# Kernel tuning notes

Measured on AMD Instinct MI355X. Metric: run time of the kernel, lower is better.

The kernel has to match this reference:

```python
import jax, jax.numpy as jnp
import numpy as np

ODE_STEPS = 4
LN_EPS = 1e-5


def setup_inputs() -> dict:
    key = jax.random.key(0)
    ks = jax.random.split(key, 18)
    B, L, F, E, H, OH = 256, 1024, 64, 128, 128, 128
    s = lambda n: 1.0 / np.sqrt(n)
    u = lambda k, shp, n: jax.random.uniform(k, shp, jnp.float32, -s(n), s(n))
    return {
        "x": jax.random.normal(ks[0], (B, L, F), jnp.float32),
        "dt": jax.random.uniform(ks[1], (B, L), jnp.float32),
        "mask": jax.random.randint(ks[2], (B, L), 0, 2).astype(jnp.int32),
        # x_proj
        "Wx": u(ks[3], (E, F), F), "bx": u(ks[4], (E,), F),
        # ODEFunc: Linear(H,OH) -> tanh -> Linear(OH,H)
        "W1": u(ks[5], (OH, H), H), "b1": u(ks[6], (OH,), H),
        "W2": u(ks[7], (H, OH), OH), "b2": u(ks[8], (H,), OH),
        # GRUCell
        "W_ih": u(ks[9], (3 * H, E), H), "b_ih": u(ks[10], (3 * H,), H),
        "W_hh": u(ks[11], (3 * H, H), H), "b_hh": u(ks[12], (3 * H,), H),
        # head: LayerNorm + Linear(H,1)
        "ln_g": jnp.ones((H,), jnp.float32), "ln_b": jnp.zeros((H,), jnp.float32),
        "Wh": u(ks[13], (1, H), H), "bh": u(ks[14], (1,), H),
    }


def reference(x, dt, Wx, bx, W1, b1, W2, b2, W_ih, b_ih, W_hh, b_hh,
              ln_g, ln_b, Wh, bh, mask):
    B, L, F = x.shape
    H = W_hh.shape[1]

    def odefunc(h):
        return jnp.tanh(h @ W1.T + b1) @ W2.T + b2

    def ode_euler(h, dte):  # dte: [B]
        step = dte / float(ODE_STEPS)
        for _ in range(ODE_STEPS):
            h = h + step[:, None] * odefunc(h)
        return h

    def gru_cell(xe, h):
        gi = xe @ W_ih.T + b_ih
        gh = h @ W_hh.T + b_hh
        i_r, i_z, i_n = jnp.split(gi, 3, axis=-1)
        h_r, h_z, h_n = jnp.split(gh, 3, axis=-1)
        r = jax.nn.sigmoid(i_r + h_r)
        z = jax.nn.sigmoid(i_z + h_z)
        n = jnp.tanh(i_n + r * h_n)
        return (1.0 - z) * n + z * h

    def step(h, inp):
        xi, dti, mi = inp  # [B,F], [B], [B] int
        mi_f = mi.astype(x.dtype)
        active = jnp.sum(mi_f) > 0  # torch skips step only if ALL masked
        hi = ode_euler(h, dti * mi_f)
        xe = jax.nn.relu(xi @ Wx.T + bx)
        hg = gru_cell(xe, hi)
        h_new = jnp.where(active, hg, h)
        return h_new, h_new

    h0 = jnp.zeros((B, H), x.dtype)
    xs = (jnp.swapaxes(x, 0, 1), dt.T, mask.T)
    _, Hs = jax.lax.scan(step, h0, xs)       # [L,B,H]
    Hs = jnp.swapaxes(Hs, 0, 1)              # [B,L,H]

    mu = jnp.mean(Hs, axis=-1, keepdims=True)
    var = jnp.var(Hs, axis=-1, keepdims=True)
    hn = (Hs - mu) / jnp.sqrt(var + LN_EPS) * ln_g + ln_b
    logits_t = (hn @ Wh.T + bh)[..., 0]      # [B,L]

    mask_f = mask.astype(x.dtype)
    logits_t = logits_t * mask_f
    len_valid = jnp.maximum(jnp.sum(mask_f, axis=1), 1.0)
    return jnp.sum(logits_t, axis=1) / len_valid
```

## Files before the change

### kernel.cpp

```cpp
#include <hip/hip_runtime.h>

#define Bb 256
#define Ll 1024
#define CH 32

typedef _Float16 h2v __attribute__((ext_vector_type(2)));

__device__ __forceinline__ unsigned pack_h2(float a, float b) {
  h2v v; v[0] = (_Float16)a; v[1] = (_Float16)b;
  return __builtin_bit_cast(unsigned, v);
}
__device__ __forceinline__ float dot2(unsigned w, unsigned x, float acc) {
#if defined(__has_builtin) && __has_builtin(__builtin_amdgcn_fdot2)
  return __builtin_amdgcn_fdot2(__builtin_bit_cast(h2v, w),
                                __builtin_bit_cast(h2v, x), acc, false);
#else
  h2v wv = __builtin_bit_cast(h2v, w), xv = __builtin_bit_cast(h2v, x);
  acc = fmaf((float)wv[0], (float)xv[0], acc);
  return fmaf((float)wv[1], (float)xv[1], acc);
#endif
}
__device__ __forceinline__ float dppadd1(float v) {
  int s = __builtin_amdgcn_mov_dpp(__builtin_bit_cast(int, v), 0xB1, 0xF, 0xF, true);
  return v + __builtin_bit_cast(float, s);
}
__device__ __forceinline__ float dppadd2(float v) {
  int s = __builtin_amdgcn_mov_dpp(__builtin_bit_cast(int, v), 0x4E, 0xF, 0xF, true);
  return v + __builtin_bit_cast(float, s);
}
__device__ __forceinline__ float qsum(float a0, float a1) {
  return dppadd2(dppadd1(a0 + a1));
}
__device__ __forceinline__ float fast_tanh(float x) {
  float e = __expf(2.0f * x);
  return 1.0f - 2.0f / (e + 1.0f);
}
__device__ __forceinline__ float fast_sigmoid(float x) {
  return 1.0f / (1.0f + __expf(-x));
}

__device__ __forceinline__ float mv16(const unsigned* __restrict__ w,
                                      const unsigned* __restrict__ v, int q0) {
  float a0 = 0.0f, a1 = 0.0f;
#pragma unroll
  for (int c = 0; c < 4; ++c) {
    const uint4 hv = *(const uint4*)&v[q0 + 4 * c];
    a0 = dot2(w[4*c+0], hv.x, a0); a1 = dot2(w[4*c+1], hv.y, a1);
    a0 = dot2(w[4*c+2], hv.z, a0); a1 = dot2(w[4*c+3], hv.w, a1);
  }
  return qsum(a0, a1);
}
__device__ __forceinline__ float giq(const unsigned* __restrict__ wrow,
                                     const unsigned* __restrict__ xe,
                                     int q0, int swi) {
  float g0 = 0.0f, g1 = 0.0f;
#pragma unroll
  for (int c = 0; c < 4; ++c) {
    const uint4 xv = *(const uint4*)&xe[q0 + 4 * c];
    const uint4 w4 = *(const uint4*)&wrow[(q0 + 4 * c) ^ swi];
    g0 = dot2(w4.x, xv.x, g0); g1 = dot2(w4.y, xv.y, g1);
    g0 = dot2(w4.z, xv.z, g0); g1 = dot2(w4.w, xv.w, g1);
  }
  return qsum(g0, g1);
}

__global__ __launch_bounds__(256) void k_prep(
    const float* __restrict__ W1, const float* __restrict__ W2,
    const float* __restrict__ b2, float* __restrict__ ws)
{
  const int idx = blockIdx.x * 256 + threadIdx.x;
  if (idx < 16384) {
    const int i = idx >> 7, j = idx & 127;
    float s = 0.f;
    for (int k = 0; k < 128; ++k) s = fmaf(W1[i * 128 + k], W2[k * 128 + j], s);
    ws[idx] = s;
  } else if (idx < 16512) {
    const int i = idx - 16384;
    float s = 0.f;
    for (int k = 0; k < 128; ++k) s = fmaf(W1[i * 128 + k], b2[k], s);
    ws[idx] = s;
  }
}

__global__ __launch_bounds__(512, 1) void k_fused(
    const float* __restrict__ x, const float* __restrict__ dtp,
    const int* __restrict__ mask,
    const float* __restrict__ Wx, const float* __restrict__ bx,
    const float* __restrict__ W1, const float* __restrict__ b1,
    const float* __restrict__ W2, const float* __restrict__ b2,
    const float* __restrict__ Wih, const float* __restrict__ bih,
    const float* __restrict__ Whh, const float* __restrict__ bhh,
    const float* __restrict__ lng, const float* __restrict__ lnb,
    const float* __restrict__ Whd, const float* __restrict__ bhp,
    const float* __restrict__ ws,
    float* __restrict__ out)
{
  const float* Mf = ws;
  const float* cf = ws + 16384;

  const int b = blockIdx.x;
  const int tid = threadIdx.x;
  const int lane = tid & 63;
  const int wv = tid >> 6;
  const int jl = lane >> 2;
  const int ks = lane & 3;
  const int j = (wv << 4) + jl;
  const int q0 = ks << 4;
  const int q0x = ks << 3;
  const int swi = (j & 15) << 2;

  __shared__ int act_lds[Ll];
  __shared__ __align__(16) unsigned wih_lds[3 * 128 * 64];
  __shared__ __align__(16) unsigned w2_lds[128 * 64];
  __shared__ __align__(16) unsigned x16[2][CH * 32];
  __shared__ __align__(16) unsigned xe16[64];
  __shared__ __align__(16) unsigned ubuf[2][64];
  __shared__ __align__(16) unsigned usumb[64];
  __shared__ __align__(16) unsigned fb16[64];
  __shared__ __align__(16) unsigned h16[2][64];
  __shared__ float dt_ch[2][CH];
  __shared__ int   m_ch[2][CH];
  __shared__ float red_lds[48];
  __shared__ float cc_lds[2];

  for (int t0 = tid; t0 < Ll; t0 += 512) {
    int a = 0;
#pragma unroll 8
    for (int bb = 0; bb < Bb; ++bb) a |= mask[(size_t)bb * Ll + t0];
    act_lds[t0] = a;
  }
  for (int idx = tid; idx < 3 * 128 * 64; idx += 512) {
    const int r = idx >> 6, w = idx & 63;
    wih_lds[(r << 6) | (w ^ ((r & 15) << 2))] =
        pack_h2(Wih[(size_t)r * 128 + 2 * w], Wih[(size_t)r * 128 + 2 * w + 1]);
  }
  for (int idx = tid; idx < 128 * 64; idx += 512) {
    const int r = idx >> 6, w = idx & 63;
    w2_lds[(r << 6) | (w ^ ((r & 15) << 2))] =
        pack_h2(W2[(size_t)r * 128 + 2 * w], W2[(size_t)r * 128 + 2 * w + 1]);
  }
  if (tid == 0) {
    float s1 = 0.f, s0 = 0.f;
    for (int i = 0; i < 128; ++i) { s1 += lng[i] * Whd[i]; s0 += lnb[i] * Whd[i]; }
    cc_lds[0] = s1; cc_lds[1] = s0 + bhp[0];
  }
  {
    const int sl = tid >> 4, part = tid & 15;
    const float4 a = *(const float4*)(x + ((size_t)b * Ll + sl) * 64 + part * 4);
    x16[0][sl * 32 + part * 2 + 0] = pack_h2(a.x, a.y);
    x16[0][sl * 32 + part * 2 + 1] = pack_h2(a.z, a.w);
    if (tid < CH) dt_ch[0][tid] = dtp[(size_t)b * Ll + tid];
    else if (tid < 2 * CH) m_ch[0][tid - CH] = mask[(size_t)b * Ll + (tid - CH)];
  }
  unsigned w1h[16], mh[16], whr[16], whz[16], whn[16], wxh[8];
#pragma unroll
  for (int ii = 0; ii < 8; ++ii) {
    float4 a4;
    a4 = *(const float4*)&W1[(size_t)j * 128 + (ks << 5) + 4 * ii];
    w1h[2*ii] = pack_h2(a4.x, a4.y); w1h[2*ii+1] = pack_h2(a4.z, a4.w);
    a4 = *(const float4*)&Mf[(size_t)j * 128 + (ks << 5) + 4 * ii];
    mh[2*ii] = pack_h2(a4.x, a4.y); mh[2*ii+1] = pack_h2(a4.z, a4.w);
    a4 = *(const float4*)&Whh[(size_t)j * 128 + (ks << 5) + 4 * ii];
    whr[2*ii] = pack_h2(a4.x, a4.y); whr[2*ii+1] = pack_h2(a4.z, a4.w);
    a4 = *(const float4*)&Whh[(size_t)(128 + j) * 128 + (ks << 5) + 4 * ii];
    whz[2*ii] = pack_h2(a4.x, a4.y); whz[2*ii+1] = pack_h2(a4.z, a4.w);
    a4 = *(const float4*)&Whh[(size_t)(256 + j) * 128 + (ks << 5) + 4 * ii];
    whn[2*ii] = pack_h2(a4.x, a4.y); whn[2*ii+1] = pack_h2(a4.z, a4.w);
  }
#pragma unroll
  for (int ii = 0; ii < 4; ++ii) {
    const float4 a4 = *(const float4*)&Wx[(size_t)j * 64 + (ks << 4) + 4 * ii];
    wxh[2*ii] = pack_h2(a4.x, a4.y); wxh[2*ii+1] = pack_h2(a4.z, a4.w);
  }
  const float bxj = bx[j], b1j = b1[j], b2j = b2[j], cj = cf[j];
  const float bir = bih[j], biz = bih[128 + j], bin_ = bih[256 + j];
  const float bhr = bhh[j], bhz = bhh[128 + j], bhn = bhh[256 + j];
  const float gw = lng[j] * Whd[j];

  if (tid < 64) { h16[0][tid] = 0u; h16[1][tid] = 0u; }
  float hreg = 0.f;
  float gicr = 0.f, gicz = 0.f, gicn = 0.f;
  float gnr = 0.f, gnz = 0.f, gnn = 0.f;
  float accb = 0.f, cntb = 0.f;
  int mreg = 0;
  float4 rx0 = {0,0,0,0}; float rdt = 0.f; int rmk = 0;
  __syncthreads();

  {
    float p0 = 0.f, p1 = 0.f;
#pragma unroll
    for (int c = 0; c < 2; ++c) {
      const uint4 xv = *(const uint4*)&x16[0][q0x + 4 * c];
      p0 = dot2(wxh[4*c+0], xv.x, p0); p1 = dot2(wxh[4*c+1], xv.y, p1);
      p0 = dot2(wxh[4*c+2], xv.z, p0); p1 = dot2(wxh[4*c+3], xv.w, p1);
    }
    const float xev = fmaxf(qsum(p0, p1) + bxj, 0.f);
    if (ks == 0) ((_Float16*)xe16)[j] = (_Float16)xev;
  }
  __syncthreads();
  gicr = giq(&wih_lds[j << 6], xe16, q0, swi) + bir;
  gicz = giq(&wih_lds[(128 + j) << 6], xe16, q0, swi) + biz;
  gicn = giq(&wih_lds[(256 + j) << 6], xe16, q0, swi) + bin_;
  __syncthreads();

#pragma unroll 1
  for (int t = 0; t < Ll; ++t) {
    const int cb = (t >> 5) & 1, tc = t & 31;
    const float sv = dt_ch[cb][tc] * (float)m_ch[cb][tc] * 0.25f;
    const unsigned* hb = h16[t & 1];
    const int refill = (tc == 16) && ((t >> 5) < 31);

    float v, usum;

    {
      if (refill) {
        const int sl = tid >> 4, part = tid & 15;
        rx0 = *(const float4*)(x + ((size_t)b * Ll + ((t >> 5) + 1) * 32 + sl) * 64 + part * 4);
        if (tid < CH) rdt = dtp[(size_t)b * Ll + ((t >> 5) + 1) * 32 + tid];
        else if (tid < 2 * CH) rmk = mask[(size_t)b * Ll + ((t >> 5) + 1) * 32 + (tid - CH)];
      }
      v = mv16(w1h, hb, q0);
      const float u0 = fast_tanh(v + b1j);
      usum = u0;
      if (ks == 0) ((_Float16*)ubuf[0])[j] = (_Float16)u0;
      if (t + 1 < Ll) {
        const int nb2 = ((t + 1) >> 5) & 1, ns = (t + 1) & 31;
        float p0 = 0.f, p1 = 0.f;
#pragma unroll
        for (int c = 0; c < 2; ++c) {
          const uint4 xv = *(const uint4*)&x16[nb2][ns * 32 + q0x + 4 * c];
          p0 = dot2(wxh[4*c+0], xv.x, p0); p1 = dot2(wxh[4*c+1], xv.y, p1);
          p0 = dot2(wxh[4*c+2], xv.z, p0); p1 = dot2(wxh[4*c+3], xv.w, p1);
        }
        const float xev = fmaxf(qsum(p0, p1) + bxj, 0.f);
        if (ks == 0) ((_Float16*)xe16)[j] = (_Float16)xev;
      }
      if (tid == 0 && t > 0) {
        float S1 = 0.f, S2 = 0.f, SD = 0.f;
#pragma unroll
        for (int q = 0; q < 16; ++q) {
          S1 += red_lds[q * 3 + 0]; S2 += red_lds[q * 3 + 1]; SD += red_lds[q * 3 + 2];
        }
        if (mreg) {
          const float mu = S1 * (1.0f / 128.0f);
          const float var = S2 * (1.0f / 128.0f) - mu * mu;
          const float rstd = rsqrtf(var + 1e-5f);
          accb += rstd * (SD - mu * cc_lds[0]) + cc_lds[1];
          cntb += 1.f;
        }
      }
    }
    __syncthreads();

    {
      const float t2 = mv16(mh, ubuf[0], q0);
      v = fmaf(sv, t2 + cj, v);
      const float u1 = fast_tanh(v + b1j);
      usum += u1;
      if (ks == 0) ((_Float16*)ubuf[1])[j] = (_Float16)u1;
      gnr = giq(&wih_lds[j << 6], xe16, q0, swi) + bir;
    }
    __syncthreads();

    {
      const float t2 = mv16(mh, ubuf[1], q0);
      v = fmaf(sv, t2 + cj, v);
      const float u2 = fast_tanh(v + b1j);
      usum += u2;
      if (ks == 0) ((_Float16*)ubuf[0])[j] = (_Float16)u2;
      gnz = giq(&wih_lds[(128 + j) << 6], xe16, q0, swi) + biz;
    }
    __syncthreads();

    {
      const float t2 = mv16(mh, ubuf[0], q0);
      v = fmaf(sv, t2 + cj, v);
      const float u3 = fast_tanh(v + b1j);
      usum += u3;
      if (ks == 0) ((_Float16*)usumb)[j] = (_Float16)usum;
      gnn = giq(&wih_lds[(256 + j) << 6], xe16, q0, swi) + bin_;
    }
    __syncthreads();

    float hf;
    {
      const float k2 = giq(&w2_lds[j << 6], usumb, q0, swi);
      hf = hreg + sv * k2 + 4.f * sv * b2j;
      if (ks == 0) ((_Float16*)fb16)[j] = (_Float16)hf;
      if (refill) {
        const int nb = ((t >> 5) + 1) & 1;
        const int sl = tid >> 4, part = tid & 15;
        x16[nb][sl * 32 + part * 2 + 0] = pack_h2(rx0.x, rx0.y);
        x16[nb][sl * 32 + part * 2 + 1] = pack_h2(rx0.z, rx0.w);
        if (tid < CH) dt_ch[nb][tid] = rdt;
        else if (tid < 2 * CH) m_ch[nb][tid - CH] = rmk;
      }
    }
    __syncthreads();

    {
      const float pr = mv16(whr, fb16, q0) + bhr;
      const float pz = mv16(whz, fb16, q0) + bhz;
      const float pn = mv16(whn, fb16, q0) + bhn;
      const float rr = fast_sigmoid(gicr + pr);
      const float zz = fast_sigmoid(gicz + pz);
      const float nn = fast_tanh(gicn + rr * pn);
      const float hg = (1.f - zz) * nn + zz * hf;
      hreg = act_lds[t] ? hg : hf;
      if (ks == 0) ((_Float16*)h16[(t + 1) & 1])[j] = (_Float16)hreg;
      float s1 = hreg, s2 = hreg * hreg, sd = hreg * gw;
#pragma unroll
      for (int o = 4; o <= 16; o <<= 1) {
        s1 += __shfl_xor(s1, o); s2 += __shfl_xor(s2, o); sd += __shfl_xor(sd, o);
      }
      if ((lane & 31) == 0) {
        const int slot = (wv << 1) | (lane >> 5);
        red_lds[slot * 3 + 0] = s1; red_lds[slot * 3 + 1] = s2; red_lds[slot * 3 + 2] = sd;
      }
      if (tid == 0) mreg = m_ch[cb][tc];
      gicr = gnr; gicz = gnz; gicn = gnn;
    }
    __syncthreads();
  }

  if (tid == 0) {
    float S1 = 0.f, S2 = 0.f, SD = 0.f;
#pragma unroll
    for (int q = 0; q < 16; ++q) {
      S1 += red_lds[q * 3 + 0]; S2 += red_lds[q * 3 + 1]; SD += red_lds[q * 3 + 2];
    }
    if (mreg) {
      const float mu = S1 * (1.0f / 128.0f);
      const float var = S2 * (1.0f / 128.0f) - mu * mu;
      const float rstd = rsqrtf(var + 1e-5f);
      accb += rstd * (SD - mu * cc_lds[0]) + cc_lds[1];
      cntb += 1.f;
    }
    out[b] = accb / fmaxf(cntb, 1.f);
  }
}

extern "C" void kernel_launch(void* const* d_in, const int* in_sizes, int n_in,
                              void* d_out, int out_size, void* d_ws, size_t ws_size,
                              hipStream_t stream) {
  const float* x    = (const float*)d_in[0];
  const float* dt   = (const float*)d_in[1];
  const int*   mask = (const int*)d_in[2];
  const float* Wx   = (const float*)d_in[3];
  const float* bx   = (const float*)d_in[4];
  const float* W1   = (const float*)d_in[5];
  const float* b1   = (const float*)d_in[6];
  const float* W2   = (const float*)d_in[7];
  const float* b2   = (const float*)d_in[8];
  const float* Wih  = (const float*)d_in[9];
  const float* bih  = (const float*)d_in[10];
  const float* Whh  = (const float*)d_in[11];
  const float* bhh  = (const float*)d_in[12];
  const float* lng  = (const float*)d_in[13];
  const float* lnb  = (const float*)d_in[14];
  const float* Wh   = (const float*)d_in[15];
  const float* bh   = (const float*)d_in[16];
  float* ws = (float*)d_ws;
  float* out = (float*)d_out;

  k_prep<<<dim3(65), dim3(256), 0, stream>>>(W1, W2, b2, ws);
  k_fused<<<dim3(Bb), dim3(512), 0, stream>>>(
      x, dt, mask, Wx, bx, W1, b1, W2, b2, Wih, bih, Whh, bhh,
      lng, lnb, Wh, bh, ws, out);
}
```

Measured before the change: 2.772 ms.

## Fold Whh into ODE update to drop a barrier and batch input-gate GEMVs per chunk

The hidden-to-hidden GRU projection is split algebraically. Whh*hf becomes Whh*h plus sv times (Whh*W2)*usum plus a bias term, using a precomputed Whh·W2 matrix and Whh·b2 vector. This removes the separate stage that wrote the post-ODE state to shared memory and its barrier, so each step has one fewer sync. The Whh*h products are computed early, overlapped with the ODE stages. Input-gate projections (Wx then Wih) are batched once per 16-step chunk from global fp16 weights into shared memory instead of being interleaved each step, and the activity flags are compressed to a bitmask. This adds more fp16 rounding and larger shared-memory use.

```diff
diff --git a/kernel.cpp b/kernel.cpp
--- a/kernel.cpp
+++ b/kernel.cpp
@@ -2,7 +2,7 @@
 
 #define Bb 256
 #define Ll 1024
-#define CH 32
+#define CH 16
 
 typedef _Float16 h2v __attribute__((ext_vector_type(2)));
 
@@ -50,24 +50,28 @@
   }
   return qsum(a0, a1);
 }
-__device__ __forceinline__ float giq(const unsigned* __restrict__ wrow,
-                                     const unsigned* __restrict__ xe,
-                                     int q0, int swi) {
-  float g0 = 0.0f, g1 = 0.0f;
+__device__ __forceinline__ void mv16x2(const unsigned* __restrict__ wA,
+                                       const unsigned* __restrict__ wB,
+                                       const unsigned* __restrict__ v, int q0,
+                                       float& rA, float& rB) {
+  float a0 = 0.f, a1 = 0.f, c0 = 0.f, c1 = 0.f;
 #pragma unroll
   for (int c = 0; c < 4; ++c) {
-    const uint4 xv = *(const uint4*)&xe[q0 + 4 * c];
-    const uint4 w4 = *(const uint4*)&wrow[(q0 + 4 * c) ^ swi];
-    g0 = dot2(w4.x, xv.x, g0); g1 = dot2(w4.y, xv.y, g1);
-    g0 = dot2(w4.z, xv.z, g0); g1 = dot2(w4.w, xv.w, g1);
-  }
-  return qsum(g0, g1);
+    const uint4 hv = *(const uint4*)&v[q0 + 4 * c];
+    a0 = dot2(wA[4*c+0], hv.x, a0); a1 = dot2(wA[4*c+1], hv.y, a1);
+    a0 = dot2(wA[4*c+2], hv.z, a0); a1 = dot2(wA[4*c+3], hv.w, a1);
+    c0 = dot2(wB[4*c+0], hv.x, c0); c1 = dot2(wB[4*c+1], hv.y, c1);
+    c0 = dot2(wB[4*c+2], hv.z, c0); c1 = dot2(wB[4*c+3], hv.w, c1);
+  }
+  rA = qsum(a0, a1); rB = qsum(c0, c1);
 }
 
 __global__ __launch_bounds__(256) void k_prep(
     const float* __restrict__ W1, const float* __restrict__ W2,
+    const float* __restrict__ Whh, const float* __restrict__ Wih,
     const float* __restrict__ b2, float* __restrict__ ws)
 {
+  unsigned* wsu = (unsigned*)ws;
   const int idx = blockIdx.x * 256 + threadIdx.x;
   if (idx < 16384) {
     const int i = idx >> 7, j = idx & 127;
@@ -79,6 +83,25 @@
     float s = 0.f;
     for (int k = 0; k < 128; ++k) s = fmaf(W1[i * 128 + k], b2[k], s);
     ws[idx] = s;
+  } else if (idx < 16896) {
+    const int r = idx - 16512;
+    float s = 0.f;
+    for (int k = 0; k < 128; ++k) s = fmaf(Whh[r * 128 + k], b2[k], s);
+    ws[idx] = s;
+  } else if (idx < 41472) {
+    const int e = idx - 16896;
+    const int r = e >> 6, w = e & 63;
+    float s0 = 0.f, s1 = 0.f;
+    for (int k = 0; k < 128; ++k) {
+      const float wh = Whh[r * 128 + k];
+      s0 = fmaf(wh, W2[k * 128 + 2 * w], s0);
+      s1 = fmaf(wh, W2[k * 128 + 2 * w + 1], s1);
+    }
+    wsu[idx] = pack_h2(s0, s1);
+  } else if (idx < 66048) {
+    const int e = idx - 41472;
+    const int r = e >> 6, w = e & 63;
+    wsu[idx] = pack_h2(Wih[r * 128 + 2 * w], Wih[r * 128 + 2 * w + 1]);
   }
 }
 
@@ -97,6 +120,10 @@
 {
   const float* Mf = ws;
   const float* cf = ws + 16384;
+  const float* df = ws + 16512;
+  const unsigned* wsu = (const unsigned*)ws;
+  const unsigned* N16 = wsu + 16896;
+  const unsigned* W16 = wsu + 41472;
 
   const int b = blockIdx.x;
   const int tid = threadIdx.x;
@@ -109,30 +136,31 @@
   const int q0x = ks << 3;
   const int swi = (j & 15) << 2;
 
-  __shared__ int act_lds[Ll];
-  __shared__ __align__(16) unsigned wih_lds[3 * 128 * 64];
+  __shared__ unsigned actb[32];
+  __shared__ __align__(16) unsigned n_lds[384 * 64];
   __shared__ __align__(16) unsigned w2_lds[128 * 64];
   __shared__ __align__(16) unsigned x16[2][CH * 32];
-  __shared__ __align__(16) unsigned xe16[64];
+  __shared__ __align__(16) unsigned xech[CH * 64];
+  __shared__ _Float16 gich[3 * CH * 128];
   __shared__ __align__(16) unsigned ubuf[2][64];
   __shared__ __align__(16) unsigned usumb[64];
-  __shared__ __align__(16) unsigned fb16[64];
   __shared__ __align__(16) unsigned h16[2][64];
   __shared__ float dt_ch[2][CH];
   __shared__ int   m_ch[2][CH];
   __shared__ float red_lds[48];
   __shared__ float cc_lds[2];
 
+  if (tid < 32) actb[tid] = 0u;
+  __syncthreads();
   for (int t0 = tid; t0 < Ll; t0 += 512) {
     int a = 0;
 #pragma unroll 8
     for (int bb = 0; bb < Bb; ++bb) a |= mask[(size_t)bb * Ll + t0];
-    act_lds[t0] = a;
-  }
-  for (int idx = tid; idx < 3 * 128 * 64; idx += 512) {
+    if (a) atomicOr(&actb[t0 >> 5], 1u << (t0 & 31));
+  }
+  for (int idx = tid; idx < 384 * 64; idx += 512) {
     const int r = idx >> 6, w = idx & 63;
-    wih_lds[(r << 6) | (w ^ ((r & 15) << 2))] =
-        pack_h2(Wih[(size_t)r * 128 + 2 * w], Wih[(size_t)r * 128 + 2 * w + 1]);
+    n_lds[(r << 6) | (w ^ ((r & 15) << 2))] = N16[idx];
   }
   for (int idx = tid; idx < 128 * 64; idx += 512) {
     const int r = idx >> 6, w = idx & 63;
@@ -145,10 +173,9 @@
     cc_lds[0] = s1; cc_lds[1] = s0 + bhp[0];
   }
   {
-    const int sl = tid >> 4, part = tid & 15;
-    const float4 a = *(const float4*)(x + ((size_t)b * Ll + sl) * 64 + part * 4);
-    x16[0][sl * 32 + part * 2 + 0] = pack_h2(a.x, a.y);
-    x16[0][sl * 32 + part * 2 + 1] = pack_h2(a.z, a.w);
+    const int sl = tid >> 5, part = tid & 31;
+    const float2 a = *(const float2*)(x + ((size_t)b * Ll + sl) * 64 + part * 2);
+    x16[0][sl * 32 + part] = pack_h2(a.x, a.y);
     if (tid < CH) dt_ch[0][tid] = dtp[(size_t)b * Ll + tid];
     else if (tid < 2 * CH) m_ch[0][tid - CH] = mask[(size_t)b * Ll + (tid - CH)];
   }
@@ -175,66 +202,67 @@
   const float bxj = bx[j], b1j = b1[j], b2j = b2[j], cj = cf[j];
   const float bir = bih[j], biz = bih[128 + j], bin_ = bih[256 + j];
   const float bhr = bhh[j], bhz = bhh[128 + j], bhn = bhh[256 + j];
+  const float ddr = df[j], ddz = df[128 + j], ddn = df[256 + j];
   const float gw = lng[j] * Whd[j];
 
   if (tid < 64) { h16[0][tid] = 0u; h16[1][tid] = 0u; }
   float hreg = 0.f;
-  float gicr = 0.f, gicz = 0.f, gicn = 0.f;
-  float gnr = 0.f, gnz = 0.f, gnn = 0.f;
   float accb = 0.f, cntb = 0.f;
   int mreg = 0;
-  float4 rx0 = {0,0,0,0}; float rdt = 0.f; int rmk = 0;
-  __syncthreads();
-
-  {
-    float p0 = 0.f, p1 = 0.f;
-#pragma unroll
-    for (int c = 0; c < 2; ++c) {
-      const uint4 xv = *(const uint4*)&x16[0][q0x + 4 * c];
-      p0 = dot2(wxh[4*c+0], xv.x, p0); p1 = dot2(wxh[4*c+1], xv.y, p1);
-      p0 = dot2(wxh[4*c+2], xv.z, p0); p1 = dot2(wxh[4*c+3], xv.w, p1);
-    }
-    const float xev = fmaxf(qsum(p0, p1) + bxj, 0.f);
-    if (ks == 0) ((_Float16*)xe16)[j] = (_Float16)xev;
-  }
-  __syncthreads();
-  gicr = giq(&wih_lds[j << 6], xe16, q0, swi) + bir;
-  gicz = giq(&wih_lds[(128 + j) << 6], xe16, q0, swi) + biz;
-  gicn = giq(&wih_lds[(256 + j) << 6], xe16, q0, swi) + bin_;
+  float2 rx0 = {0, 0}; float rdt = 0.f; int rmk = 0;
   __syncthreads();
 
 #pragma unroll 1
   for (int t = 0; t < Ll; ++t) {
-    const int cb = (t >> 5) & 1, tc = t & 31;
-    const float sv = dt_ch[cb][tc] * (float)m_ch[cb][tc] * 0.25f;
-    const unsigned* hb = h16[t & 1];
-    const int refill = (tc == 16) && ((t >> 5) < 31);
-
-    float v, usum;
-
-    {
-      if (refill) {
-        const int sl = tid >> 4, part = tid & 15;
-        rx0 = *(const float4*)(x + ((size_t)b * Ll + ((t >> 5) + 1) * 32 + sl) * 64 + part * 4);
-        if (tid < CH) rdt = dtp[(size_t)b * Ll + ((t >> 5) + 1) * 32 + tid];
-        else if (tid < 2 * CH) rmk = mask[(size_t)b * Ll + ((t >> 5) + 1) * 32 + (tid - CH)];
-      }
-      v = mv16(w1h, hb, q0);
-      const float u0 = fast_tanh(v + b1j);
-      usum = u0;
-      if (ks == 0) ((_Float16*)ubuf[0])[j] = (_Float16)u0;
-      if (t + 1 < Ll) {
-        const int nb2 = ((t + 1) >> 5) & 1, ns = (t + 1) & 31;
+    const int cb = (t >> 4) & 1, tc = t & 15;
+
+    if (tc == 0) {
+#pragma unroll 1
+      for (int tp = 0; tp < CH; ++tp) {
         float p0 = 0.f, p1 = 0.f;
 #pragma unroll
         for (int c = 0; c < 2; ++c) {
-          const uint4 xv = *(const uint4*)&x16[nb2][ns * 32 + q0x + 4 * c];
+          const uint4 xv = *(const uint4*)&x16[cb][tp * 32 + q0x + 4 * c];
           p0 = dot2(wxh[4*c+0], xv.x, p0); p1 = dot2(wxh[4*c+1], xv.y, p1);
           p0 = dot2(wxh[4*c+2], xv.z, p0); p1 = dot2(wxh[4*c+3], xv.w, p1);
         }
         const float xev = fmaxf(qsum(p0, p1) + bxj, 0.f);
-        if (ks == 0) ((_Float16*)xe16)[j] = (_Float16)xev;
-      }
+        if (ks == 0) ((_Float16*)xech)[tp * 128 + j] = (_Float16)xev;
+      }
+      __syncthreads();
+#pragma unroll 1
+      for (int g = 0; g < 3; ++g) {
+        unsigned wihs[16];
+        const uint4* wp = (const uint4*)(W16 + ((size_t)(g * 128 + j) << 6) + (ks << 4));
+#pragma unroll
+        for (int i = 0; i < 4; ++i) *(uint4*)&wihs[4 * i] = wp[i];
+        const float bg = (g == 0) ? bir : (g == 1) ? biz : bin_;
+#pragma unroll 1
+        for (int tp = 0; tp < CH; ++tp) {
+          const float gv = mv16(wihs, &xech[tp * 64], q0);
+          if (ks == 0) gich[(g * CH + tp) * 128 + j] = (_Float16)(gv + bg);
+        }
+      }
+      __syncthreads();
+    }
+
+    const float sv = dt_ch[cb][tc] * (float)m_ch[cb][tc] * 0.25f;
+    const unsigned* hb = h16[t & 1];
+    const int refill = (tc == 8) && ((t >> 4) < 63);
+
+    float v, usum, whr0, whz0, whn0;
+
+    {
+      if (refill) {
+        const int sl = tid >> 5, part = tid & 31;
+        rx0 = *(const float2*)(x + ((size_t)b * Ll + ((t >> 4) + 1) * CH + sl) * 64 + part * 2);
+        if (tid < CH) rdt = dtp[(size_t)b * Ll + ((t >> 4) + 1) * CH + tid];
+        else if (tid < 2 * CH) rmk = mask[(size_t)b * Ll + ((t >> 4) + 1) * CH + (tid - CH)];
+      }
+      mv16x2(w1h, whr, hb, q0, v, whr0);
+      const float u0 = fast_tanh(v + b1j);
+      usum = u0;
+      if (ks == 0) ((_Float16*)ubuf[0])[j] = (_Float16)u0;
       if (tid == 0 && t > 0) {
         float S1 = 0.f, S2 = 0.f, SD = 0.f;
 #pragma unroll
@@ -254,21 +282,21 @@
 
     {
       const float t2 = mv16(mh, ubuf[0], q0);
+      whz0 = mv16(whz, hb, q0);
       v = fmaf(sv, t2 + cj, v);
       const float u1 = fast_tanh(v + b1j);
       usum += u1;
       if (ks == 0) ((_Float16*)ubuf[1])[j] = (_Float16)u1;
-      gnr = giq(&wih_lds[j << 6], xe16, q0, swi) + bir;
     }
     __syncthreads();
 
     {
       const float t2 = mv16(mh, ubuf[1], q0);
+      whn0 = mv16(whn, hb, q0);
       v = fmaf(sv, t2 + cj, v);
       const float u2 = fast_tanh(v + b1j);
       usum += u2;
       if (ks == 0) ((_Float16*)ubuf[0])[j] = (_Float16)u2;
-      gnz = giq(&wih_lds[(128 + j) << 6], xe16, q0, swi) + biz;
     }
     __syncthreads();
 
@@ -278,35 +306,51 @@
       const float u3 = fast_tanh(v + b1j);
       usum += u3;
       if (ks == 0) ((_Float16*)usumb)[j] = (_Float16)usum;
-      gnn = giq(&wih_lds[(256 + j) << 6], xe16, q0, swi) + bin_;
     }
     __syncthreads();
 
-    float hf;
     {
-      const float k2 = giq(&w2_lds[j << 6], usumb, q0, swi);
-      hf = hreg + sv * k2 + 4.f * sv * b2j;
-      if (ks == 0) ((_Float16*)fb16)[j] = (_Float16)hf;
-      if (refill) {
-        const int nb = ((t >> 5) + 1) & 1;
-        const int sl = tid >> 4, part = tid & 15;
-        x16[nb][sl * 32 + part * 2 + 0] = pack_h2(rx0.x, rx0.y);
-        x16[nb][sl * 32 + part * 2 + 1] = pack_h2(rx0.z, rx0.w);
-        if (tid < CH) dt_ch[nb][tid] = rdt;
-        else if (tid < 2 * CH) m_ch[nb][tid - CH] = rmk;
-      }
-    }
-    __syncthreads();
-
-    {
-      const float pr = mv16(whr, fb16, q0) + bhr;
-      const float pz = mv16(whz, fb16, q0) + bhz;
-      const float pn = mv16(whn, fb16, q0) + bhn;
-      const float rr = fast_sigmoid(gicr + pr);
-      const float zz = fast_sigmoid(gicz + pz);
-      const float nn = fast_tanh(gicn + rr * pn);
-      const float hg = (1.f - zz) * nn + zz * hf;
-      hreg = act_lds[t] ? hg : hf;
+      float k2a = 0.f, k2b = 0.f, kra = 0.f, krb = 0.f;
+      float kza = 0.f, kzb = 0.f, kna = 0.f, knb = 0.f;
+      const unsigned* w2r = &w2_lds[j << 6];
+      const unsigned* nrr = &n_lds[j << 6];
+      const unsigned* nzr = &n_lds[(128 + j) << 6];
+      const unsigned* nnr = &n_lds[(256 + j) << 6];
+#pragma unroll
+      for (int c = 0; c < 4; ++c) {
+        const int off = (q0 + 4 * c) ^ swi;
+        const uint4 uv = *(const uint4*)&usumb[q0 + 4 * c];
+        const uint4 wa = *(const uint4*)&w2r[off];
+        k2a = dot2(wa.x, uv.x, k2a); k2b = dot2(wa.y, uv.y, k2b);
+        k2a = dot2(wa.z, uv.z, k2a); k2b = dot2(wa.w, uv.w, k2b);
+        const uint4 wb = *(const uint4*)&nrr[off];
+        kra = dot2(wb.x, uv.x, kra); krb = dot2(wb.y, uv.y, krb);
+        kra = dot2(wb.z, uv.z, kra); krb = dot2(wb.w, uv.w, krb);
+        const uint4 wc = *(const uint4*)&nzr[off];
+        kza = dot2(wc.x, uv.x, kza); kzb = dot2(wc.y, uv.y, kzb);
+        kza = dot2(wc.z, uv.z, kza); kzb = dot2(wc.w, uv.w, kzb);
+        const uint4 wd = *(const uint4*)&nnr[off];
+        kna = dot2(wd.x, uv.x, kna); knb = dot2(wd.y, uv.y, knb);
+        kna = dot2(wd.z, uv.z, kna); knb = dot2(wd.w, uv.w, knb);
+      }
+      const float k2 = qsum(k2a, k2b);
+      const float kr = qsum(kra, krb);
+      const float kz = qsum(kza, kzb);
+      const float kn = qsum(kna, knb);
+      const float sv4 = 4.f * sv;
+      const float hf = hreg + sv * k2 + sv4 * b2j;
+      const float prer = whr0 + sv * kr + sv4 * ddr + bhr;
+      const float prez = whz0 + sv * kz + sv4 * ddz + bhz;
+      const float pren = whn0 + sv * kn + sv4 * ddn + bhn;
+      const float gir = (float)gich[(0 * CH + tc) * 128 + j];
+      const float giz = (float)gich[(1 * CH + tc) * 128 + j];
+      const float gin = (float)gich[(2 * CH + tc) * 128 + j];
+      const float rr = fast_sigmoid(gir + prer);
+      const float zz = fast_sigmoid(giz + prez);
+      const float gn_ = fast_tanh(gin + rr * pren);
+      const float hg = (1.f - zz) * gn_ + zz * hf;
+      const int actv = (actb[t >> 5] >> (t & 31)) & 1;
+      hreg = actv ? hg : hf;
       if (ks == 0) ((_Float16*)h16[(t + 1) & 1])[j] = (_Float16)hreg;
       float s1 = hreg, s2 = hreg * hreg, sd = hreg * gw;
 #pragma unroll
@@ -318,7 +362,13 @@
         red_lds[slot * 3 + 0] = s1; red_lds[slot * 3 + 1] = s2; red_lds[slot * 3 + 2] = sd;
       }
       if (tid == 0) mreg = m_ch[cb][tc];
-      gicr = gnr; gicz = gnz; gicn = gnn;
+      if (refill) {
+        const int nb = ((t >> 4) + 1) & 1;
+        const int sl = tid >> 5, part = tid & 31;
+        x16[nb][sl * 32 + part] = pack_h2(rx0.x, rx0.y);
+        if (tid < CH) dt_ch[nb][tid] = rdt;
+        else if (tid < 2 * CH) m_ch[nb][tid - CH] = rmk;
+      }
     }
     __syncthreads();
   }
@@ -363,7 +413,7 @@
   float* ws = (float*)d_ws;
   float* out = (float*)d_out;
 
-  k_prep<<<dim3(65), dim3(256), 0, stream>>>(W1, W2, b2, ws);
+  k_prep<<<dim3(258), dim3(256), 0, stream>>>(W1, W2, Whh, Wih, b2, ws);
   k_fused<<<dim3(Bb), dim3(512), 0, stream>>>(
       x, dt, mask, Wx, bx, W1, b1, W2, b2, Wih, bih, Whh, bhh,
       lng, lnb, Wh, bh, ws, out);
```

After: 3.131 ms. +12.9%, slower.
